# Optimization experiments

Hardware: AMD Instinct MI355X
Metric: run time of the kernel (lower is better)

The kernel has to match this reference:

```python
import jax, jax.numpy as jnp
import numpy as np

B, L, K, D, S = 8, 1024, 1024, 128, 16  # batch, nodes, eigvecs, d_model(=d_inner), d_state
ABAR_EPS = 1e-3
BN_EPS = 1e-5


def setup_inputs() -> dict:
    key = jax.random.key(0)
    ks = jax.random.split(key, 10)
    x = jax.random.normal(ks[0], (B, L, D), jnp.float32)
    attn_mask = jnp.ones((B, L), jnp.bool_)
    EigVecs = jax.random.normal(ks[1], (B, L, K), jnp.float32)
    EigVals = jax.random.uniform(ks[2], (B, K), jnp.float32)
    # BatchNorm1d (eval mode) params
    bn_gamma = jnp.ones((D,), jnp.float32)
    bn_beta = jnp.zeros((D,), jnp.float32)
    bn_mean = jnp.zeros((D,), jnp.float32)
    bn_var = jnp.ones((D,), jnp.float32)
    # in_proj Linear(D, 2*D)
    W_in = jax.random.normal(ks[3], (D, 2 * D), jnp.float32) / np.float32(np.sqrt(D))
    b_in = jnp.zeros((2 * D,), jnp.float32)
    # SSM params
    log_Delta = np.float32(np.log(1e-3)) + np.float32(np.log(0.1) - np.log(1e-3)) * jax.random.uniform(ks[4], (1, D), jnp.float32)
    Bp = 0.01 * jax.random.normal(ks[5], (1, D, S), jnp.float32)
    Cp = 0.01 * jax.random.normal(ks[6], (1, D, S), jnp.float32)
    log_A_real = jnp.log(0.5 * jnp.ones((D, S), jnp.float32))
    A_imag = jnp.pi * jnp.broadcast_to(jnp.arange(D, dtype=jnp.float32)[:, None], (D, S))
    # out_proj Linear(D, D)
    W_out = jax.random.normal(ks[7], (D, D), jnp.float32) / np.float32(np.sqrt(D))
    b_out = jnp.zeros((D,), jnp.float32)
    return {
        "x": x, "attn_mask": attn_mask, "EigVecs": EigVecs, "EigVals": EigVals,
        "bn_gamma": bn_gamma, "bn_beta": bn_beta, "bn_mean": bn_mean, "bn_var": bn_var,
        "W_in": W_in, "b_in": b_in, "log_Delta": log_Delta, "Bp": Bp, "Cp": Cp,
        "log_A_real": log_A_real, "A_imag": A_imag, "W_out": W_out, "b_out": b_out,
    }


def reference(x, attn_mask, EigVecs, EigVals, bn_gamma, bn_beta, bn_mean, bn_var,
              W_in, b_in, log_Delta, Bp, Cp, log_A_real, A_imag, W_out, b_out):
    # --- eig preprocessing ---
    ev = 1.0 - EigVals[:, :, None, None]            # (B,K,1,1)
    ev = jnp.nan_to_num(ev)
    Q = jnp.nan_to_num(EigVecs)                      # (B,L,K)
    Q = Q / jnp.linalg.norm(Q, axis=-1, keepdims=True)
    Q = jnp.nan_to_num(Q)
    # --- in_proj: BatchNorm1d (eval) + Linear ---
    xb = (x - bn_mean) * (bn_gamma / jnp.sqrt(bn_var + BN_EPS)) + bn_beta
    h = xb @ W_in + b_in                             # (B,L,2D)
    x1, z = jnp.split(h, 2, axis=-1)                 # split [d_model, d_model]
    u = x1 * jax.nn.silu(z)                          # (B,L,D)
    # --- discretized SSM params ---
    delta = jnp.exp(log_Delta)                       # (1,D)
    A = -jnp.exp(log_A_real) + 1j * A_imag           # (D,S) complex
    Abar = jnp.exp(-ABAR_EPS + delta[..., None] * A) # (1,D,S) complex
    Bbar = delta[..., None] * Bp                     # (1,D,S)
    # --- graph Fourier transform ---
    QTX = jnp.einsum('blk,bld->bkd', Q, u)           # (B,K,D)
    QTXB = QTX[..., None] * Bbar                     # (B,K,D,S)
    lamA = ev * Abar[:, None]                        # (B,K,D,S) complex
    lamQ = jnp.real(lamA / (1.0 - lamA) * QTXB)      # A_complex & not BC_complex -> .real
    # --- inverse transform + C reduction (fused) ---
    yssm = jnp.einsum('blk,bkds,ds->bld', Q, lamQ, Cp[0])  # (B,L,D)
    y = jax.nn.silu(yssm) @ W_out + b_out
    return y
```

## Files before the change

kernel.cpp:

```cpp
#include <hip/hip_runtime.h>
#include <math.h>

#define B_ 8
#define L_ 1024
#define K_ 1024
#define D_ 128
#define S_ 16
#define DS_ (D_ * S_)
#define NIT_ 16

typedef short bf16x8 __attribute__((ext_vector_type(8)));
typedef float f32x4 __attribute__((ext_vector_type(4)));
typedef __attribute__((address_space(1))) const unsigned int gu32;
typedef __attribute__((address_space(3))) unsigned int lu32;

__device__ inline unsigned short f2bf(float f) {
    unsigned int u = __float_as_uint(f);
    u = (u + 0x7fffu + ((u >> 16) & 1u)) >> 16;
    return (unsigned short)u;
}
__device__ inline float bf2f(unsigned short h) {
    return __uint_as_float(((unsigned int)h) << 16);
}

__device__ inline size_t bswz(int b, int c, int n) {
    return ((((size_t)b * 32 + (c >> 5)) * 4 + ((c >> 3) & 3)) * 128 + n) * 8;
}

__global__ __launch_bounds__(256) void k_pre(
    const float* __restrict__ E, const float* __restrict__ x,
    const float* __restrict__ g, const float* __restrict__ beta,
    const float* __restrict__ mean, const float* __restrict__ var,
    const float* __restrict__ W_in, const float* __restrict__ b_in,
    const float* __restrict__ log_Delta, const float* __restrict__ Bp,
    const float* __restrict__ Cp, const float* __restrict__ log_A_real,
    const float* __restrict__ A_imag,
    float* __restrict__ rn_out, float* __restrict__ par,
    unsigned short* __restrict__ uswH, unsigned short* __restrict__ uswL) {
    __shared__ float xb[16][128];
    __shared__ float rsum[16];
    __shared__ float rnS[16];
    int bx = blockIdx.x;
    int row0 = bx * 16;
    int t = threadIdx.x;
    if (bx < 8) {
        int i = bx * 256 + t;
        int d = i >> 4, s = i & 15;
        double delta = exp((double)log_Delta[d]);
        double Are = -exp((double)log_A_real[i]);
        double Aim = (double)A_imag[i];
        double mag = exp(-1e-3 + delta * Are);
        double ang = delta * Aim;
        int o = s * D_ + d;
        par[o]           = (float)(mag * cos(ang));
        par[DS_ + o]     = (float)(mag * sin(ang));
        par[2 * DS_ + o] = (float)(delta * (double)Bp[i] * (double)Cp[i]);
    }
    {
        int r = t >> 4, tt = t & 15;
        const float4* Ep = (const float4*)(E + (size_t)(row0 + r) * K_);
        float s = 0.f;
        #pragma unroll
        for (int i = 0; i < 16; ++i) {
            float4 v = Ep[tt + i * 16];
            s += v.x * v.x + v.y * v.y + v.z * v.z + v.w * v.w;
        }
        s += __shfl_xor(s, 8, 64);
        s += __shfl_xor(s, 4, 64);
        s += __shfl_xor(s, 2, 64);
        s += __shfl_xor(s, 1, 64);
        if (tt == 0) rsum[r] = s;
    }
    #pragma unroll
    for (int p = 0; p < 8; ++p) {
        int idx = t + p * 256;
        int dd = idx & 127, r = idx >> 7;
        float sc = g[dd] / sqrtf(var[dd] + 1e-5f);
        xb[r][dd] = (x[(size_t)(row0 + r) * D_ + dd] - mean[dd]) * sc + beta[dd];
    }
    __syncthreads();
    if (t < 16) {
        float rv = 1.0f / sqrtf(rsum[t]);
        rnS[t] = rv;
        rn_out[row0 + t] = rv;
    }
    __syncthreads();
    int j = t & 127, half = t >> 7;
    float acc1[8], acc2[8];
    #pragma unroll
    for (int r = 0; r < 8; ++r) { acc1[r] = 0.f; acc2[r] = 0.f; }
    #pragma unroll 4
    for (int dd = 0; dd < 128; ++dd) {
        float w1 = W_in[dd * 256 + j];
        float w2 = W_in[dd * 256 + 128 + j];
        #pragma unroll
        for (int r = 0; r < 8; ++r) {
            float xv = xb[half * 8 + r][dd];
            acc1[r] = fmaf(xv, w1, acc1[r]);
            acc2[r] = fmaf(xv, w2, acc2[r]);
        }
    }
    float b1 = b_in[j], b2 = b_in[128 + j];
    bf16x8 hv, lv;
    #pragma unroll
    for (int r = 0; r < 8; ++r) {
        int rr = half * 8 + r;
        float x1 = acc1[r] + b1;
        float z  = acc2[r] + b2;
        float sig = 1.0f / (1.0f + __expf(-z));
        float uv = rnS[rr] * x1 * z * sig;
        unsigned short h = f2bf(uv);
        hv[r] = (short)h;
        lv[r] = (short)f2bf(uv - bf2f(h));
    }
    int b = row0 >> 10;
    int l0 = (row0 & 1023) + half * 8;
    size_t off = bswz(b, l0, j);
    *(bf16x8*)&uswH[off] = hv;
    *(bf16x8*)&uswL[off] = lv;
}

#define STAGE_B(itS, nb)                                                        \
    _Pragma("unroll")                                                           \
    for (int j2 = 0; j2 < 8; ++j2) {                                            \
        int s = wave + j2 * 4;                                      \
        int cts = s >> 4, s2 = s & 15;                                          \
        int qq = s2 & 3, nh = (s2 >> 2) & 1, hl = s2 >> 3;                      \
        size_t src0 = (size_t)((itS) * 2 + cts) * 4096;                         \
        const unsigned short* src =                                             \
            (hl ? BbL : BbH) + src0 + ((size_t)qq * 128 + nh * 64 + lane) * 8;  \
        unsigned short* dst =                                                   \
            (hl ? &sBl[nb][cts][0] : &sBh[nb][cts][0]) + qq * 1032 + nh * 512;  \
        __builtin_amdgcn_global_load_lds((gu32*)src, (lu32*)dst, 16, 0, 0);     \
    }

#define G1_WRITE_A(nb, v0, v1, v2, v3)                                           \
    {                                                                            \
        unsigned short h0 = f2bf(v0), h1 = f2bf(v1);                             \
        unsigned short l0 = f2bf((v0) - bf2f(h0)), l1 = f2bf((v1) - bf2f(h1));   \
        *(unsigned int*)&sAh[nb][0][aoff] = (unsigned)h0 | ((unsigned)h1 << 16); \
        *(unsigned int*)&sAl[nb][0][aoff] = (unsigned)l0 | ((unsigned)l1 << 16); \
        unsigned short h2 = f2bf(v2), h3 = f2bf(v3);                             \
        unsigned short l2 = f2bf((v2) - bf2f(h2)), l3 = f2bf((v3) - bf2f(h3));   \
        *(unsigned int*)&sAh[nb][1][aoff] = (unsigned)h2 | ((unsigned)h3 << 16); \
        *(unsigned int*)&sAl[nb][1][aoff] = (unsigned)l2 | ((unsigned)l3 << 16); \
    }

__global__ __launch_bounds__(256) void k_g1(
    const float* __restrict__ E,
    const unsigned short* __restrict__ BH, const unsigned short* __restrict__ BL,
    const float* __restrict__ EigVals, const float* __restrict__ par,
    unsigned short* __restrict__ GswH, unsigned short* __restrict__ GswL) {
    __shared__ alignas(16) unsigned short sAh[2][2][640], sAl[2][2][640];
    __shared__ alignas(16) unsigned short sBh[2][2][4128], sBl[2][2][4128];
    __shared__ float evS[16];
    int bx = blockIdx.x;
    int b = bx & 7;
    int m0 = (bx >> 3) * 16;
    const float* Ab = E + (size_t)b * (1024 * 1024);
    const unsigned short* BbH = BH + (size_t)b * 131072;
    const unsigned short* BbL = BL + (size_t)b * 131072;
    int t = threadIdx.x;
    int wave = t >> 6, lane = t & 63;
    int fr = lane & 15, q = lane >> 4;
    int wn = wave * 32;
    int am = t & 15, jj = t >> 4;
    int ag = jj >> 2;
    int arot = (ag + (am >> 3)) & 3;
    int aoff = am * 40 + arot * 8 + ((2 * jj) & 7);
    if (t < 16) evS[t] = 1.0f - EigVals[b * 1024 + m0 + t];
    f32x4 acc[2];
    acc[0] = (f32x4){0.f, 0.f, 0.f, 0.f};
    acc[1] = (f32x4){0.f, 0.f, 0.f, 0.f};

    {
        float v0 = Ab[(size_t)(2 * jj) * 1024 + m0 + am];
        float v1 = Ab[(size_t)(2 * jj + 1) * 1024 + m0 + am];
        float v2 = Ab[(size_t)(32 + 2 * jj) * 1024 + m0 + am];
        float v3 = Ab[(size_t)(32 + 2 * jj + 1) * 1024 + m0 + am];
        STAGE_B(0, 0);
        G1_WRITE_A(0, v0, v1, v2, v3);
        asm volatile("s_waitcnt vmcnt(0) lgkmcnt(0)" ::: "memory");
        __builtin_amdgcn_s_barrier();
    }

    #pragma unroll 2
    for (int it = 0; it < NIT_; ++it) {
        int buf = it & 1, nb = buf ^ 1;
        float v0 = 0.f, v1 = 0.f, v2 = 0.f, v3 = 0.f;
        if (it + 1 < NIT_) {
            int cb = (it + 1) * 64;
            v0 = Ab[(size_t)(cb + 2 * jj) * 1024 + m0 + am];
            v1 = Ab[(size_t)(cb + 2 * jj + 1) * 1024 + m0 + am];
            v2 = Ab[(size_t)(cb + 32 + 2 * jj) * 1024 + m0 + am];
            v3 = Ab[(size_t)(cb + 32 + 2 * jj + 1) * 1024 + m0 + am];
            STAGE_B(it + 1, nb);
        }
        __builtin_amdgcn_s_setprio(1);
        #pragma unroll
        for (int ks = 0; ks < 2; ++ks) {
            bf16x8 ah, al, bh[2], bl[2];
            {
                int p = (q + (fr >> 3)) & 3;
                int off = fr * 40 + p * 8;
                ah = *(const bf16x8*)&sAh[buf][ks][off];
                al = *(const bf16x8*)&sAl[buf][ks][off];
            }
            #pragma unroll
            for (int nt = 0; nt < 2; ++nt) {
                int off = q * 1032 + (wn + nt * 16 + fr) * 8;
                bh[nt] = *(const bf16x8*)&sBh[buf][ks][off];
                bl[nt] = *(const bf16x8*)&sBl[buf][ks][off];
            }
            #pragma unroll
            for (int nt = 0; nt < 2; ++nt) {
                acc[nt] = __builtin_amdgcn_mfma_f32_16x16x32_bf16(ah, bh[nt], acc[nt], 0, 0, 0);
                acc[nt] = __builtin_amdgcn_mfma_f32_16x16x32_bf16(ah, bl[nt], acc[nt], 0, 0, 0);
                acc[nt] = __builtin_amdgcn_mfma_f32_16x16x32_bf16(al, bh[nt], acc[nt], 0, 0, 0);
            }
        }
        __builtin_amdgcn_s_setprio(0);
        if (it + 1 < NIT_) G1_WRITE_A(nb, v0, v1, v2, v3);
        asm volatile("s_waitcnt vmcnt(0) lgkmcnt(0)" ::: "memory");
        __builtin_amdgcn_s_barrier();
    }

    float (*Gs)[132] = (float (*)[132])(&sBh[0][0][0]);
    #pragma unroll
    for (int nt = 0; nt < 2; ++nt) {
        int col = wn + nt * 16 + fr;
        #pragma unroll
        for (int r = 0; r < 4; ++r)
            Gs[q * 4 + r][col] = acc[nt][r];
    }
    __syncthreads();
    {
        int col = t & 127, rowg = t >> 7;
        float arr[S_], aii[S_], ccc[S_];
        #pragma unroll
        for (int ss = 0; ss < S_; ++ss) {
            arr[ss] = par[ss * D_ + col];
            aii[ss] = par[DS_ + ss * D_ + col];
            ccc[ss] = par[2 * DS_ + ss * D_ + col];
        }
        #pragma unroll
        for (int i = 0; i < 8; ++i) {
            int row = rowg * 8 + i;
            float ev = evS[row];
            float w = 0.f;
            #pragma unroll
            for (int ss = 0; ss < S_; ++ss) {
                float a = ev * arr[ss], bi = ev * aii[ss];
                float oma = 1.0f - a;
                float b2 = bi * bi;
                float num = fmaf(a, oma, -b2);
                float den = fmaf(oma, oma, b2);
                float rr = __builtin_amdgcn_rcpf(den);
                rr = rr * (2.0f - den * rr);
                w = fmaf(ccc[ss], num * rr, w);
            }
            Gs[row][col] *= w;
        }
    }
    __syncthreads();
    {
        int d = t & 127, kg = t >> 7;
        bf16x8 hv, lv;
        #pragma unroll
        for (int i = 0; i < 8; ++i) {
            float v = Gs[kg * 8 + i][d];
            unsigned short h = f2bf(v);
            hv[i] = (short)h;
            lv[i] = (short)f2bf(v - bf2f(h));
        }
        int ct = m0 >> 5;
        int qsel = ((m0 >> 3) & 2) + kg;
        size_t off = (((size_t)(b * 32 + ct) * 4 + qsel) * 128 + d) * 8;
        *(bf16x8*)&GswH[off] = hv;
        *(bf16x8*)&GswL[off] = lv;
    }
}

__global__ __launch_bounds__(256) void k_g2(
    const float* __restrict__ E,
    const unsigned short* __restrict__ BH, const unsigned short* __restrict__ BL,
    const float* __restrict__ rn, const float* __restrict__ W_out,
    const float* __restrict__ b_out, float* __restrict__ y) {
    __shared__ alignas(16) unsigned short sAh[2][2][640], sAl[2][2][640];
    __shared__ alignas(16) unsigned short sBh[2][2][4128], sBl[2][2][4128];
    __shared__ float rnS[16];
    int bx = blockIdx.x;
    int b = bx & 7;
    int m0 = (bx >> 3) * 16;
    const float* Ab = E + (size_t)b * (1024 * 1024);
    const unsigned short* BbH = BH + (size_t)b * 131072;
    const unsigned short* BbL = BL + (size_t)b * 131072;
    int t = threadIdx.x;
    int wave = t >> 6, lane = t & 63;
    int fr = lane & 15, q = lane >> 4;
    int wn = wave * 32;
    int am = t >> 4, c4 = (t & 15) * 4;
    int chunk = c4 >> 5, cw = c4 & 31;
    int ag = cw >> 3;
    int arot = (ag + (am >> 3)) & 3;
    int aoff = am * 40 + arot * 8 + (cw & 7);
    if (t < 16) rnS[t] = rn[b * 1024 + m0 + t];
    f32x4 acc[2];
    acc[0] = (f32x4){0.f, 0.f, 0.f, 0.f};
    acc[1] = (f32x4){0.f, 0.f, 0.f, 0.f};

#define G2_WRITE_A(nb, va)                                                       \
    {                                                                            \
        unsigned short h0 = f2bf((va).x), h1 = f2bf((va).y);                     \
        unsigned short h2 = f2bf((va).z), h3 = f2bf((va).w);                     \
        unsigned short l0 = f2bf((va).x - bf2f(h0)), l1 = f2bf((va).y - bf2f(h1));\
        unsigned short l2 = f2bf((va).z - bf2f(h2)), l3 = f2bf((va).w - bf2f(h3));\
        *(uint2*)&sAh[nb][chunk][aoff] =                                         \
            (uint2){(unsigned)h0 | ((unsigned)h1 << 16),                         \
                    (unsigned)h2 | ((unsigned)h3 << 16)};                        \
        *(uint2*)&sAl[nb][chunk][aoff] =                                         \
            (uint2){(unsigned)l0 | ((unsigned)l1 << 16),                         \
                    (unsigned)l2 | ((unsigned)l3 << 16)};                        \
    }

    {
        float4 va = *(const float4*)&Ab[(size_t)(m0 + am) * 1024 + c4];
        STAGE_B(0, 0);
        G2_WRITE_A(0, va);
        asm volatile("s_waitcnt vmcnt(0) lgkmcnt(0)" ::: "memory");
        __builtin_amdgcn_s_barrier();
    }

    #pragma unroll 2
    for (int it = 0; it < NIT_; ++it) {
        int buf = it & 1, nb = buf ^ 1;
        float4 va = (float4){0.f, 0.f, 0.f, 0.f};
        if (it + 1 < NIT_) {
            int cb = (it + 1) * 64;
            va = *(const float4*)&Ab[(size_t)(m0 + am) * 1024 + cb + c4];
            STAGE_B(it + 1, nb);
        }
        __builtin_amdgcn_s_setprio(1);
        #pragma unroll
        for (int ks = 0; ks < 2; ++ks) {
            bf16x8 ah, al, bh[2], bl[2];
            {
                int p = (q + (fr >> 3)) & 3;
                int off = fr * 40 + p * 8;
                ah = *(const bf16x8*)&sAh[buf][ks][off];
                al = *(const bf16x8*)&sAl[buf][ks][off];
            }
            #pragma unroll
            for (int nt = 0; nt < 2; ++nt) {
                int off = q * 1032 + (wn + nt * 16 + fr) * 8;
                bh[nt] = *(const bf16x8*)&sBh[buf][ks][off];
                bl[nt] = *(const bf16x8*)&sBl[buf][ks][off];
            }
            #pragma unroll
            for (int nt = 0; nt < 2; ++nt) {
                acc[nt] = __builtin_amdgcn_mfma_f32_16x16x32_bf16(ah, bh[nt], acc[nt], 0, 0, 0);
                acc[nt] = __builtin_amdgcn_mfma_f32_16x16x32_bf16(ah, bl[nt], acc[nt], 0, 0, 0);
                acc[nt] = __builtin_amdgcn_mfma_f32_16x16x32_bf16(al, bh[nt], acc[nt], 0, 0, 0);
            }
        }
        __builtin_amdgcn_s_setprio(0);
        if (it + 1 < NIT_) G2_WRITE_A(nb, va);
        asm volatile("s_waitcnt vmcnt(0) lgkmcnt(0)" ::: "memory");
        __builtin_amdgcn_s_barrier();
    }

    float (*Ys)[132] = (float (*)[132])(&sBh[0][0][0]);
    #pragma unroll
    for (int nt = 0; nt < 2; ++nt) {
        int col = wn + nt * 16 + fr;
        #pragma unroll
        for (int r = 0; r < 4; ++r) {
            int row = q * 4 + r;
            float v = acc[nt][r] * rnS[row];
            float sig = 1.0f / (1.0f + __expf(-v));
            Ys[row][col] = v * sig;
        }
    }
    __syncthreads();
    int j = t & 127, h = t >> 7;
    float a2[8];
    #pragma unroll
    for (int r = 0; r < 8; ++r) a2[r] = 0.f;
    for (int dd = 0; dd < 128; dd += 4) {
        float w0 = W_out[(dd + 0) * 128 + j];
        float w1 = W_out[(dd + 1) * 128 + j];
        float w2 = W_out[(dd + 2) * 128 + j];
        float w3 = W_out[(dd + 3) * 128 + j];
        #pragma unroll
        for (int r = 0; r < 8; ++r) {
            float4 yv = *(float4*)&Ys[h * 8 + r][dd];
            a2[r] = fmaf(yv.x, w0, a2[r]);
            a2[r] = fmaf(yv.y, w1, a2[r]);
            a2[r] = fmaf(yv.z, w2, a2[r]);
            a2[r] = fmaf(yv.w, w3, a2[r]);
        }
    }
    float bo = b_out[j];
    #pragma unroll
    for (int r = 0; r < 8; ++r)
        y[((size_t)b * 1024 + m0 + h * 8 + r) * 128 + j] = a2[r] + bo;
}

extern "C" void kernel_launch(void* const* d_in, const int* in_sizes, int n_in,
                              void* d_out, int out_size, void* d_ws, size_t ws_size,
                              hipStream_t stream) {
    const float* x          = (const float*)d_in[0];
    const float* EigVecs    = (const float*)d_in[2];
    const float* EigVals    = (const float*)d_in[3];
    const float* bn_gamma   = (const float*)d_in[4];
    const float* bn_beta    = (const float*)d_in[5];
    const float* bn_mean    = (const float*)d_in[6];
    const float* bn_var     = (const float*)d_in[7];
    const float* W_in       = (const float*)d_in[8];
    const float* b_in       = (const float*)d_in[9];
    const float* log_Delta  = (const float*)d_in[10];
    const float* Bp         = (const float*)d_in[11];
    const float* Cp         = (const float*)d_in[12];
    const float* log_A_real = (const float*)d_in[13];
    const float* A_imag     = (const float*)d_in[14];
    const float* W_out      = (const float*)d_in[15];
    const float* b_out      = (const float*)d_in[16];

    float* y = (float*)d_out;
    char* w = (char*)d_ws;
    float* rn            = (float*)(w);
    float* par           = (float*)(w + 32768);
    unsigned short* uswH = (unsigned short*)(w + 65536);
    unsigned short* uswL = (unsigned short*)(w + 65536 + (1u << 21));
    unsigned short* GswH = (unsigned short*)(w + 65536 + 2 * (1u << 21));
    unsigned short* GswL = (unsigned short*)(w + 65536 + 3 * (1u << 21));

    k_pre<<<dim3(B_ * L_ / 16), dim3(256), 0, stream>>>(
        EigVecs, x, bn_gamma, bn_beta, bn_mean, bn_var, W_in, b_in,
        log_Delta, Bp, Cp, log_A_real, A_imag, rn, par, uswH, uswL);
    k_g1<<<dim3(512), dim3(256), 0, stream>>>(
        EigVecs, uswH, uswL, EigVals, par, GswH, GswL);
    k_g2<<<dim3(512), dim3(256), 0, stream>>>(
        EigVecs, GswH, GswL, rn, W_out, b_out, y);
}
```

Baseline: 167.8 us.

## Prefetch GEMM tiles two iterations ahead via registers instead of direct-to-LDS loads

Replaces the global_load_lds staging of B tiles in both GEMM kernels with register-staged loads issued two iterations ahead, then written to LDS after the MFMA compute. The A tile loads use the same two-deep register ring. The per-iteration vmcnt(0) wait is removed so global loads overlap with more compute, and the barrier moves before the compute. It also adds launch_bounds(256,2) for occupancy. The cost is much higher register use (16 extra bf16x8 vectors), which may cause spills under the occupancy constraint, plus an extra LDS write pass through VGPRs.

```diff
diff --git a/kernel.cpp b/kernel.cpp
--- a/kernel.cpp
+++ b/kernel.cpp
@@ -11,8 +11,6 @@
 
 typedef short bf16x8 __attribute__((ext_vector_type(8)));
 typedef float f32x4 __attribute__((ext_vector_type(4)));
-typedef __attribute__((address_space(1))) const unsigned int gu32;
-typedef __attribute__((address_space(3))) unsigned int lu32;
 
 __device__ inline unsigned short f2bf(float f) {
     unsigned int u = __float_as_uint(f);
@@ -120,18 +118,25 @@
     *(bf16x8*)&uswL[off] = lv;
 }
 
-#define STAGE_B(itS, nb)                                                        \
-    _Pragma("unroll")                                                           \
-    for (int j2 = 0; j2 < 8; ++j2) {                                            \
-        int s = wave + j2 * 4;                                      \
-        int cts = s >> 4, s2 = s & 15;                                          \
-        int qq = s2 & 3, nh = (s2 >> 2) & 1, hl = s2 >> 3;                      \
-        size_t src0 = (size_t)((itS) * 2 + cts) * 4096;                         \
-        const unsigned short* src =                                             \
-            (hl ? BbL : BbH) + src0 + ((size_t)qq * 128 + nh * 64 + lane) * 8;  \
-        unsigned short* dst =                                                   \
-            (hl ? &sBl[nb][cts][0] : &sBh[nb][cts][0]) + qq * 1032 + nh * 512;  \
-        __builtin_amdgcn_global_load_lds((gu32*)src, (lu32*)dst, 16, 0, 0);     \
+#define LOAD_B(s, tl)                                                     \
+    {                                                                     \
+        const bf16x8* pH = (const bf16x8*)(BbH + (size_t)(tl) * 8192);    \
+        const bf16x8* pL = (const bf16x8*)(BbL + (size_t)(tl) * 8192);    \
+        _Pragma("unroll")                                                 \
+        for (int k = 0; k < 4; ++k) {                                     \
+            rBH[s][k] = pH[t + k * 256];                                  \
+            rBL[s][k] = pL[t + k * 256];                                  \
+        }                                                                 \
+    }
+#define WRITE_B(s, nb)                                                    \
+    {                                                                     \
+        char* dH = (char*)&sBh[nb][0][0];                                 \
+        char* dL = (char*)&sBl[nb][0][0];                                 \
+        _Pragma("unroll")                                                 \
+        for (int k = 0; k < 4; ++k) {                                     \
+            *(bf16x8*)(dH + ldsb[k]) = rBH[s][k];                         \
+            *(bf16x8*)(dL + ldsb[k]) = rBL[s][k];                         \
+        }                                                                 \
     }
 
 #define G1_WRITE_A(nb, v0, v1, v2, v3)                                           \
@@ -146,7 +151,16 @@
         *(unsigned int*)&sAl[nb][1][aoff] = (unsigned)l2 | ((unsigned)l3 << 16); \
     }
 
-__global__ __launch_bounds__(256) void k_g1(
+#define G1_LOAD_A(s, tl)                                                  \
+    {                                                                     \
+        int cb_ = (tl) * 64;                                              \
+        rA[s][0] = Ab[(size_t)(cb_ + 2 * jj) * 1024 + m0 + am];           \
+        rA[s][1] = Ab[(size_t)(cb_ + 2 * jj + 1) * 1024 + m0 + am];       \
+        rA[s][2] = Ab[(size_t)(cb_ + 32 + 2 * jj) * 1024 + m0 + am];      \
+        rA[s][3] = Ab[(size_t)(cb_ + 32 + 2 * jj + 1) * 1024 + m0 + am];  \
+    }
+
+__global__ __launch_bounds__(256, 2) void k_g1(
     const float* __restrict__ E,
     const unsigned short* __restrict__ BH, const unsigned short* __restrict__ BL,
     const float* __restrict__ EigVals, const float* __restrict__ par,
@@ -169,33 +183,32 @@
     int arot = (ag + (am >> 3)) & 3;
     int aoff = am * 40 + arot * 8 + ((2 * jj) & 7);
     if (t < 16) evS[t] = 1.0f - EigVals[b * 1024 + m0 + t];
+    unsigned ldsb[4];
+    #pragma unroll
+    for (int k = 0; k < 4; ++k) {
+        int gg = t + k * 256;
+        ldsb[k] = (unsigned)((gg >> 9) * 8256 + ((gg >> 7) & 3) * 2064 + (gg & 127) * 16);
+    }
+    bf16x8 rBH[2][4], rBL[2][4];
+    float rA[2][4];
     f32x4 acc[2];
     acc[0] = (f32x4){0.f, 0.f, 0.f, 0.f};
     acc[1] = (f32x4){0.f, 0.f, 0.f, 0.f};
 
-    {
-        float v0 = Ab[(size_t)(2 * jj) * 1024 + m0 + am];
-        float v1 = Ab[(size_t)(2 * jj + 1) * 1024 + m0 + am];
-        float v2 = Ab[(size_t)(32 + 2 * jj) * 1024 + m0 + am];
-        float v3 = Ab[(size_t)(32 + 2 * jj + 1) * 1024 + m0 + am];
-        STAGE_B(0, 0);
-        G1_WRITE_A(0, v0, v1, v2, v3);
-        asm volatile("s_waitcnt vmcnt(0) lgkmcnt(0)" ::: "memory");
-        __builtin_amdgcn_s_barrier();
-    }
+    G1_LOAD_A(0, 0); LOAD_B(0, 0);
+    G1_LOAD_A(1, 1); LOAD_B(1, 1);
+    G1_WRITE_A(0, rA[0][0], rA[0][1], rA[0][2], rA[0][3]);
+    WRITE_B(0, 0);
+    asm volatile("s_waitcnt lgkmcnt(0)" ::: "memory");
 
     #pragma unroll 2
     for (int it = 0; it < NIT_; ++it) {
         int buf = it & 1, nb = buf ^ 1;
-        float v0 = 0.f, v1 = 0.f, v2 = 0.f, v3 = 0.f;
-        if (it + 1 < NIT_) {
-            int cb = (it + 1) * 64;
-            v0 = Ab[(size_t)(cb + 2 * jj) * 1024 + m0 + am];
-            v1 = Ab[(size_t)(cb + 2 * jj + 1) * 1024 + m0 + am];
-            v2 = Ab[(size_t)(cb + 32 + 2 * jj) * 1024 + m0 + am];
-            v3 = Ab[(size_t)(cb + 32 + 2 * jj + 1) * 1024 + m0 + am];
-            STAGE_B(it + 1, nb);
-        }
+        int sI = it & 1, sC = sI ^ 1;
+        if (it + 2 < NIT_) { G1_LOAD_A(sI, it + 2); LOAD_B(sI, it + 2); }
+        asm volatile("" ::: "memory");
+        __builtin_amdgcn_s_barrier();
+        asm volatile("" ::: "memory");
         __builtin_amdgcn_s_setprio(1);
         #pragma unroll
         for (int ks = 0; ks < 2; ++ks) {
@@ -220,9 +233,11 @@
             }
         }
         __builtin_amdgcn_s_setprio(0);
-        if (it + 1 < NIT_) G1_WRITE_A(nb, v0, v1, v2, v3);
-        asm volatile("s_waitcnt vmcnt(0) lgkmcnt(0)" ::: "memory");
-        __builtin_amdgcn_s_barrier();
+        if (it + 1 < NIT_) {
+            G1_WRITE_A(nb, rA[sC][0], rA[sC][1], rA[sC][2], rA[sC][3]);
+            WRITE_B(sC, nb);
+            asm volatile("s_waitcnt lgkmcnt(0)" ::: "memory");
+        }
     }
 
     float (*Gs)[132] = (float (*)[132])(&sBh[0][0][0]);
@@ -281,7 +296,21 @@
     }
 }
 
-__global__ __launch_bounds__(256) void k_g2(
+#define G2_WRITE_A(nb, va)                                                       \
+    {                                                                            \
+        unsigned short h0 = f2bf((va).x), h1 = f2bf((va).y);                     \
+        unsigned short h2 = f2bf((va).z), h3 = f2bf((va).w);                     \
+        unsigned short l0 = f2bf((va).x - bf2f(h0)), l1 = f2bf((va).y - bf2f(h1));\
+        unsigned short l2 = f2bf((va).z - bf2f(h2)), l3 = f2bf((va).w - bf2f(h3));\
+        *(uint2*)&sAh[nb][chunk][aoff] =                                         \
+            (uint2){(unsigned)h0 | ((unsigned)h1 << 16),                         \
+                    (unsigned)h2 | ((unsigned)h3 << 16)};                        \
+        *(uint2*)&sAl[nb][chunk][aoff] =                                         \
+            (uint2){(unsigned)l0 | ((unsigned)l1 << 16),                         \
+                    (unsigned)l2 | ((unsigned)l3 << 16)};                        \
+    }
+
+__global__ __launch_bounds__(256, 2) void k_g2(
     const float* __restrict__ E,
     const unsigned short* __restrict__ BH, const unsigned short* __restrict__ BL,
     const float* __restrict__ rn, const float* __restrict__ W_out,
@@ -305,41 +334,35 @@
     int arot = (ag + (am >> 3)) & 3;
     int aoff = am * 40 + arot * 8 + (cw & 7);
     if (t < 16) rnS[t] = rn[b * 1024 + m0 + t];
+    unsigned ldsb[4];
+    #pragma unroll
+    for (int k = 0; k < 4; ++k) {
+        int gg = t + k * 256;
+        ldsb[k] = (unsigned)((gg >> 9) * 8256 + ((gg >> 7) & 3) * 2064 + (gg & 127) * 16);
+    }
+    bf16x8 rBH[2][4], rBL[2][4];
+    float4 rA4[2];
     f32x4 acc[2];
     acc[0] = (f32x4){0.f, 0.f, 0.f, 0.f};
     acc[1] = (f32x4){0.f, 0.f, 0.f, 0.f};
 
-#define G2_WRITE_A(nb, va)                                                       \
-    {                                                                            \
-        unsigned short h0 = f2bf((va).x), h1 = f2bf((va).y);                     \
-        unsigned short h2 = f2bf((va).z), h3 = f2bf((va).w);                     \
-        unsigned short l0 = f2bf((va).x - bf2f(h0)), l1 = f2bf((va).y - bf2f(h1));\
-        unsigned short l2 = f2bf((va).z - bf2f(h2)), l3 = f2bf((va).w - bf2f(h3));\
-        *(uint2*)&sAh[nb][chunk][aoff] =                                         \
-            (uint2){(unsigned)h0 | ((unsigned)h1 << 16),                         \
-                    (unsigned)h2 | ((unsigned)h3 << 16)};                        \
-        *(uint2*)&sAl[nb][chunk][aoff] =                                         \
-            (uint2){(unsigned)l0 | ((unsigned)l1 << 16),                         \
-                    (unsigned)l2 | ((unsigned)l3 << 16)};                        \
-    }
-
-    {
-        float4 va = *(const float4*)&Ab[(size_t)(m0 + am) * 1024 + c4];
-        STAGE_B(0, 0);
-        G2_WRITE_A(0, va);
-        asm volatile("s_waitcnt vmcnt(0) lgkmcnt(0)" ::: "memory");
-        __builtin_amdgcn_s_barrier();
-    }
+#define G2_LOAD_A(s, tl)                                                         \
+    rA4[s] = *(const float4*)&Ab[(size_t)(m0 + am) * 1024 + (tl) * 64 + c4];
+
+    G2_LOAD_A(0, 0); LOAD_B(0, 0);
+    G2_LOAD_A(1, 1); LOAD_B(1, 1);
+    G2_WRITE_A(0, rA4[0]);
+    WRITE_B(0, 0);
+    asm volatile("s_waitcnt lgkmcnt(0)" ::: "memory");
 
     #pragma unroll 2
     for (int it = 0; it < NIT_; ++it) {
         int buf = it & 1, nb = buf ^ 1;
-        float4 va = (float4){0.f, 0.f, 0.f, 0.f};
-        if (it + 1 < NIT_) {
-            int cb = (it + 1) * 64;
-            va = *(const float4*)&Ab[(size_t)(m0 + am) * 1024 + cb + c4];
-            STAGE_B(it + 1, nb);
-        }
+        int sI = it & 1, sC = sI ^ 1;
+        if (it + 2 < NIT_) { G2_LOAD_A(sI, it + 2); LOAD_B(sI, it + 2); }
+        asm volatile("" ::: "memory");
+        __builtin_amdgcn_s_barrier();
+        asm volatile("" ::: "memory");
         __builtin_amdgcn_s_setprio(1);
         #pragma unroll
         for (int ks = 0; ks < 2; ++ks) {
@@ -364,9 +387,11 @@
             }
         }
         __builtin_amdgcn_s_setprio(0);
-        if (it + 1 < NIT_) G2_WRITE_A(nb, va);
-        asm volatile("s_waitcnt vmcnt(0) lgkmcnt(0)" ::: "memory");
-        __builtin_amdgcn_s_barrier();
+        if (it + 1 < NIT_) {
+            G2_WRITE_A(nb, rA4[sC]);
+            WRITE_B(sC, nb);
+            asm volatile("s_waitcnt lgkmcnt(0)" ::: "memory");
+        }
     }
 
     float (*Ys)[132] = (float (*)[132])(&sBh[0][0][0]);
```

Measured after the change: 167.2 us. Within noise of the previous version (-0.4%).

## Enlarge GEMM tiles to 32 rows with 512 threads and triple-buffer B prefetch

Applied to the files above, without the earlier changes.

Both GEMM kernels now process 32 rows of the eigenvector matrix per block using 8 waves arranged 2x4. This halves the grid and doubles reuse of each staged B tile. B tiles are triple-buffered and prefetched two iterations ahead, so the per-iteration wait covers only LDS traffic rather than all global loads. The costs are more LDS per block and fewer blocks. The epilogue and the G layout indexing are also adjusted to the new 32-row tile.

```diff
diff --git a/kernel.cpp b/kernel.cpp
--- a/kernel.cpp
+++ b/kernel.cpp
@@ -122,8 +122,8 @@
 
 #define STAGE_B(itS, nb)                                                        \
     _Pragma("unroll")                                                           \
-    for (int j2 = 0; j2 < 8; ++j2) {                                            \
-        int s = wave + j2 * 4;                                      \
+    for (int j2 = 0; j2 < 4; ++j2) {                                            \
+        int s = wave * 4 + j2;                         \
         int cts = s >> 4, s2 = s & 15;                                          \
         int qq = s2 & 3, nh = (s2 >> 2) & 1, hl = s2 >> 3;                      \
         size_t src0 = (size_t)((itS) * 2 + cts) * 4096;                         \
@@ -146,47 +146,78 @@
         *(unsigned int*)&sAl[nb][1][aoff] = (unsigned)l2 | ((unsigned)l3 << 16); \
     }
 
-__global__ __launch_bounds__(256) void k_g1(
+#define MFMA_PHASE(aB, cB)                                                       \
+    __builtin_amdgcn_s_setprio(1);                                               \
+    _Pragma("unroll")                                                            \
+    for (int ks = 0; ks < 2; ++ks) {                                             \
+        bf16x8 ah, al, bh[2], bl[2];                                             \
+        {                                                                        \
+            int row = wm * 16 + fr;                                              \
+            int p = (q + (row >> 3)) & 3;                                        \
+            int offA = row * 40 + p * 8;                                         \
+            ah = *(const bf16x8*)&sAh[aB][ks][offA];                             \
+            al = *(const bf16x8*)&sAl[aB][ks][offA];                             \
+        }                                                                        \
+        _Pragma("unroll")                                                        \
+        for (int nt = 0; nt < 2; ++nt) {                                         \
+            int offB = q * 1032 + (wn + nt * 16 + fr) * 8;                       \
+            bh[nt] = *(const bf16x8*)&sBh[cB][ks][offB];                         \
+            bl[nt] = *(const bf16x8*)&sBl[cB][ks][offB];                         \
+        }                                                                        \
+        _Pragma("unroll")                                                        \
+        for (int nt = 0; nt < 2; ++nt) {                                         \
+            acc[nt] = __builtin_amdgcn_mfma_f32_16x16x32_bf16(ah, bh[nt], acc[nt], 0, 0, 0); \
+            acc[nt] = __builtin_amdgcn_mfma_f32_16x16x32_bf16(ah, bl[nt], acc[nt], 0, 0, 0); \
+            acc[nt] = __builtin_amdgcn_mfma_f32_16x16x32_bf16(al, bh[nt], acc[nt], 0, 0, 0); \
+        }                                                                        \
+    }                                                                            \
+    __builtin_amdgcn_s_setprio(0);
+
+__global__ __launch_bounds__(512, 2) void k_g1(
     const float* __restrict__ E,
     const unsigned short* __restrict__ BH, const unsigned short* __restrict__ BL,
     const float* __restrict__ EigVals, const float* __restrict__ par,
     unsigned short* __restrict__ GswH, unsigned short* __restrict__ GswL) {
-    __shared__ alignas(16) unsigned short sAh[2][2][640], sAl[2][2][640];
-    __shared__ alignas(16) unsigned short sBh[2][2][4128], sBl[2][2][4128];
-    __shared__ float evS[16];
+    __shared__ alignas(16) unsigned short sAh[2][2][1280], sAl[2][2][1280];
+    __shared__ alignas(16) unsigned short sBh[3][2][4128], sBl[3][2][4128];
+    __shared__ float evS[32];
     int bx = blockIdx.x;
     int b = bx & 7;
-    int m0 = (bx >> 3) * 16;
+    int m0 = (bx >> 3) * 32;
     const float* Ab = E + (size_t)b * (1024 * 1024);
     const unsigned short* BbH = BH + (size_t)b * 131072;
     const unsigned short* BbL = BL + (size_t)b * 131072;
     int t = threadIdx.x;
     int wave = t >> 6, lane = t & 63;
     int fr = lane & 15, q = lane >> 4;
-    int wn = wave * 32;
-    int am = t & 15, jj = t >> 4;
+    int wm = wave & 1;
+    int wn = (wave >> 1) * 32;
+    int am = t & 31, jj = t >> 5;
     int ag = jj >> 2;
     int arot = (ag + (am >> 3)) & 3;
     int aoff = am * 40 + arot * 8 + ((2 * jj) & 7);
-    if (t < 16) evS[t] = 1.0f - EigVals[b * 1024 + m0 + t];
+    if (t < 32) evS[t] = 1.0f - EigVals[b * 1024 + m0 + t];
     f32x4 acc[2];
     acc[0] = (f32x4){0.f, 0.f, 0.f, 0.f};
     acc[1] = (f32x4){0.f, 0.f, 0.f, 0.f};
 
     {
+        STAGE_B(0, 0);
+        STAGE_B(1, 1);
         float v0 = Ab[(size_t)(2 * jj) * 1024 + m0 + am];
         float v1 = Ab[(size_t)(2 * jj + 1) * 1024 + m0 + am];
         float v2 = Ab[(size_t)(32 + 2 * jj) * 1024 + m0 + am];
         float v3 = Ab[(size_t)(32 + 2 * jj + 1) * 1024 + m0 + am];
-        STAGE_B(0, 0);
         G1_WRITE_A(0, v0, v1, v2, v3);
         asm volatile("s_waitcnt vmcnt(0) lgkmcnt(0)" ::: "memory");
         __builtin_amdgcn_s_barrier();
-    }
-
-    #pragma unroll 2
+        asm volatile("" ::: "memory");
+    }
+
     for (int it = 0; it < NIT_; ++it) {
-        int buf = it & 1, nb = buf ^ 1;
+        int cB = it % 3;
+        int fB = (it + 2) % 3;
+        int aB = it & 1, naB = aB ^ 1;
         float v0 = 0.f, v1 = 0.f, v2 = 0.f, v3 = 0.f;
         if (it + 1 < NIT_) {
             int cb = (it + 1) * 64;
@@ -194,35 +225,13 @@
             v1 = Ab[(size_t)(cb + 2 * jj + 1) * 1024 + m0 + am];
             v2 = Ab[(size_t)(cb + 32 + 2 * jj) * 1024 + m0 + am];
             v3 = Ab[(size_t)(cb + 32 + 2 * jj + 1) * 1024 + m0 + am];
-            STAGE_B(it + 1, nb);
-        }
-        __builtin_amdgcn_s_setprio(1);
-        #pragma unroll
-        for (int ks = 0; ks < 2; ++ks) {
-            bf16x8 ah, al, bh[2], bl[2];
-            {
-                int p = (q + (fr >> 3)) & 3;
-                int off = fr * 40 + p * 8;
-                ah = *(const bf16x8*)&sAh[buf][ks][off];
-                al = *(const bf16x8*)&sAl[buf][ks][off];
-            }
-            #pragma unroll
-            for (int nt = 0; nt < 2; ++nt) {
-                int off = q * 1032 + (wn + nt * 16 + fr) * 8;
-                bh[nt] = *(const bf16x8*)&sBh[buf][ks][off];
-                bl[nt] = *(const bf16x8*)&sBl[buf][ks][off];
-            }
-            #pragma unroll
-            for (int nt = 0; nt < 2; ++nt) {
-                acc[nt] = __builtin_amdgcn_mfma_f32_16x16x32_bf16(ah, bh[nt], acc[nt], 0, 0, 0);
-                acc[nt] = __builtin_amdgcn_mfma_f32_16x16x32_bf16(ah, bl[nt], acc[nt], 0, 0, 0);
-                acc[nt] = __builtin_amdgcn_mfma_f32_16x16x32_bf16(al, bh[nt], acc[nt], 0, 0, 0);
-            }
-        }
-        __builtin_amdgcn_s_setprio(0);
-        if (it + 1 < NIT_) G1_WRITE_A(nb, v0, v1, v2, v3);
-        asm volatile("s_waitcnt vmcnt(0) lgkmcnt(0)" ::: "memory");
+        }
+        if (it + 2 < NIT_) STAGE_B(it + 2, fB);
+        MFMA_PHASE(aB, cB)
+        if (it + 1 < NIT_) G1_WRITE_A(naB, v0, v1, v2, v3);
+        asm volatile("s_waitcnt lgkmcnt(0)" ::: "memory");
         __builtin_amdgcn_s_barrier();
+        asm volatile("" ::: "memory");
     }
 
     float (*Gs)[132] = (float (*)[132])(&sBh[0][0][0]);
@@ -231,7 +240,7 @@
         int col = wn + nt * 16 + fr;
         #pragma unroll
         for (int r = 0; r < 4; ++r)
-            Gs[q * 4 + r][col] = acc[nt][r];
+            Gs[wm * 16 + q * 4 + r][col] = acc[nt][r];
     }
     __syncthreads();
     {
@@ -274,40 +283,11 @@
             lv[i] = (short)f2bf(v - bf2f(h));
         }
         int ct = m0 >> 5;
-        int qsel = ((m0 >> 3) & 2) + kg;
-        size_t off = (((size_t)(b * 32 + ct) * 4 + qsel) * 128 + d) * 8;
+        size_t off = (((size_t)(b * 32 + ct) * 4 + kg) * 128 + d) * 8;
         *(bf16x8*)&GswH[off] = hv;
         *(bf16x8*)&GswL[off] = lv;
     }
 }
-
-__global__ __launch_bounds__(256) void k_g2(
-    const float* __restrict__ E,
-    const unsigned short* __restrict__ BH, const unsigned short* __restrict__ BL,
-    const float* __restrict__ rn, const float* __restrict__ W_out,
-    const float* __restrict__ b_out, float* __restrict__ y) {
-    __shared__ alignas(16) unsigned short sAh[2][2][640], sAl[2][2][640];
-    __shared__ alignas(16) unsigned short sBh[2][2][4128], sBl[2][2][4128];
-    __shared__ float rnS[16];
-    int bx = blockIdx.x;
-    int b = bx & 7;
-    int m0 = (bx >> 3) * 16;
-    const float* Ab = E + (size_t)b * (1024 * 1024);
-    const unsigned short* BbH = BH + (size_t)b * 131072;
-    const unsigned short* BbL = BL + (size_t)b * 131072;
-    int t = threadIdx.x;
-    int wave = t >> 6, lane = t & 63;
-    int fr = lane & 15, q = lane >> 4;
-    int wn = wave * 32;
-    int am = t >> 4, c4 = (t & 15) * 4;
-    int chunk = c4 >> 5, cw = c4 & 31;
-    int ag = cw >> 3;
-    int arot = (ag + (am >> 3)) & 3;
-    int aoff = am * 40 + arot * 8 + (cw & 7);
-    if (t < 16) rnS[t] = rn[b * 1024 + m0 + t];
-    f32x4 acc[2];
-    acc[0] = (f32x4){0.f, 0.f, 0.f, 0.f};
-    acc[1] = (f32x4){0.f, 0.f, 0.f, 0.f};
 
 #define G2_WRITE_A(nb, va)                                                       \
     {                                                                            \
@@ -323,50 +303,58 @@
                     (unsigned)l2 | ((unsigned)l3 << 16)};                        \
     }
 
+__global__ __launch_bounds__(512, 2) void k_g2(
+    const float* __restrict__ E,
+    const unsigned short* __restrict__ BH, const unsigned short* __restrict__ BL,
+    const float* __restrict__ rn, const float* __restrict__ W_out,
+    const float* __restrict__ b_out, float* __restrict__ y) {
+    __shared__ alignas(16) unsigned short sAh[2][2][1280], sAl[2][2][1280];
+    __shared__ alignas(16) unsigned short sBh[3][2][4128], sBl[3][2][4128];
+    __shared__ float rnS[32];
+    int bx = blockIdx.x;
+    int b = bx & 7;
+    int m0 = (bx >> 3) * 32;
+    const float* Ab = E + (size_t)b * (1024 * 1024);
+    const unsigned short* BbH = BH + (size_t)b * 131072;
+    const unsigned short* BbL = BL + (size_t)b * 131072;
+    int t = threadIdx.x;
+    int wave = t >> 6, lane = t & 63;
+    int fr = lane & 15, q = lane >> 4;
+    int wm = wave & 1;
+    int wn = (wave >> 1) * 32;
+    int am = t >> 4, c4 = (t & 15) * 4;
+    int chunk = c4 >> 5, cw = c4 & 31;
+    int ag = cw >> 3;
+    int arot = (ag + (am >> 3)) & 3;
+    int aoff = am * 40 + arot * 8 + (cw & 7);
+    if (t < 32) rnS[t] = rn[b * 1024 + m0 + t];
+    f32x4 acc[2];
+    acc[0] = (f32x4){0.f, 0.f, 0.f, 0.f};
+    acc[1] = (f32x4){0.f, 0.f, 0.f, 0.f};
+
     {
+        STAGE_B(0, 0);
+        STAGE_B(1, 1);
         float4 va = *(const float4*)&Ab[(size_t)(m0 + am) * 1024 + c4];
-        STAGE_B(0, 0);
         G2_WRITE_A(0, va);
         asm volatile("s_waitcnt vmcnt(0) lgkmcnt(0)" ::: "memory");
         __builtin_amdgcn_s_barrier();
-    }
-
-    #pragma unroll 2
+        asm volatile("" ::: "memory");
+    }
+
     for (int it = 0; it < NIT_; ++it) {
-        int buf = it & 1, nb = buf ^ 1;
+        int cB = it % 3;
+        int fB = (it + 2) % 3;
+        int aB = it & 1, naB = aB ^ 1;
         float4 va = (float4){0.f, 0.f, 0.f, 0.f};
-        if (it + 1 < NIT_) {
-            int cb = (it + 1) * 64;
-            va = *(const float4*)&Ab[(size_t)(m0 + am) * 1024 + cb + c4];
-            STAGE_B(it + 1, nb);
-        }
-        __builtin_amdgcn_s_setprio(1);
-        #pragma unroll
-        for (int ks = 0; ks < 2; ++ks) {
-            bf16x8 ah, al, bh[2], bl[2];
-            {
-                int p = (q + (fr >> 3)) & 3;
-                int off = fr * 40 + p * 8;
-                ah = *(const bf16x8*)&sAh[buf][ks][off];
-                al = *(const bf16x8*)&sAl[buf][ks][off];
-            }
-            #pragma unroll
-            for (int nt = 0; nt < 2; ++nt) {
-                int off = q * 1032 + (wn + nt * 16 + fr) * 8;
-                bh[nt] = *(const bf16x8*)&sBh[buf][ks][off];
-                bl[nt] = *(const bf16x8*)&sBl[buf][ks][off];
-            }
-            #pragma unroll
-            for (int nt = 0; nt < 2; ++nt) {
-                acc[nt] = __builtin_amdgcn_mfma_f32_16x16x32_bf16(ah, bh[nt], acc[nt], 0, 0, 0);
-                acc[nt] = __builtin_amdgcn_mfma_f32_16x16x32_bf16(ah, bl[nt], acc[nt], 0, 0, 0);
-                acc[nt] = __builtin_amdgcn_mfma_f32_16x16x32_bf16(al, bh[nt], acc[nt], 0, 0, 0);
-            }
-        }
-        __builtin_amdgcn_s_setprio(0);
-        if (it + 1 < NIT_) G2_WRITE_A(nb, va);
-        asm volatile("s_waitcnt vmcnt(0) lgkmcnt(0)" ::: "memory");
+        if (it + 1 < NIT_)
+            va = *(const float4*)&Ab[(size_t)(m0 + am) * 1024 + (it + 1) * 64 + c4];
+        if (it + 2 < NIT_) STAGE_B(it + 2, fB);
+        MFMA_PHASE(aB, cB)
+        if (it + 1 < NIT_) G2_WRITE_A(naB, va);
+        asm volatile("s_waitcnt lgkmcnt(0)" ::: "memory");
         __builtin_amdgcn_s_barrier();
+        asm volatile("" ::: "memory");
     }
 
     float (*Ys)[132] = (float (*)[132])(&sBh[0][0][0]);
@@ -375,7 +363,7 @@
         int col = wn + nt * 16 + fr;
         #pragma unroll
         for (int r = 0; r < 4; ++r) {
-            int row = q * 4 + r;
+            int row = wm * 16 + q * 4 + r;
             float v = acc[nt][r] * rnS[row];
             float sig = 1.0f / (1.0f + __expf(-v));
             Ys[row][col] = v * sig;
@@ -438,8 +426,8 @@
     k_pre<<<dim3(B_ * L_ / 16), dim3(256), 0, stream>>>(
         EigVecs, x, bn_gamma, bn_beta, bn_mean, bn_var, W_in, b_in,
         log_Delta, Bp, Cp, log_A_real, A_imag, rn, par, uswH, uswL);
-    k_g1<<<dim3(512), dim3(256), 0, stream>>>(
+    k_g1<<<dim3(256), dim3(512), 0, stream>>>(
         EigVecs, uswH, uswL, EigVals, par, GswH, GswL);
-    k_g2<<<dim3(512), dim3(256), 0, stream>>>(
+    k_g2<<<dim3(256), dim3(512), 0, stream>>>(
         EigVecs, GswH, GswL, rn, W_out, b_out, y);
 }
```

After: 164.0 us. 1.02x faster.
